# Kernel optimization log

Hardware: AMD Instinct MI355X
Metric: run time of the kernel (lower is better)

Reference implementation:

```python
import jax, jax.numpy as jnp
import numpy as np

N = 2048      # nodes
E = 65536     # edges (avg degree 32)
NV = 6        # n_views (edge_attr dim)
C1, C2, C3 = 32, 32, 32


def _nnconv(x, edge_index, edge_attr, W, b, root, bias, in_c, out_c):
    # Edge MLP: Linear(n_views, in*out) + ReLU -> per-edge weight matrix [E, in, out]
    w = jax.nn.relu(edge_attr @ W + b).reshape(-1, in_c, out_c)
    src, dst = edge_index[0], edge_index[1]  # source_to_target flow
    msg = jnp.einsum('ei,eio->eo', x[src], w)          # gather + edge-specific matmul
    summed = jax.ops.segment_sum(msg, dst, num_segments=N)
    cnt = jax.ops.segment_sum(jnp.ones((msg.shape[0],), x.dtype), dst, num_segments=N)
    agg = summed / jnp.maximum(cnt, 1.0)[:, None]       # scatter-mean (0 for isolated nodes)
    return agg + x @ root + bias                        # root weight + bias (PyG NNConv defaults)


def setup_inputs() -> dict:
    key = jax.random.key(0)
    ks = jax.random.split(key, 12)
    s = 0.1
    return {
        'x': jax.random.normal(ks[0], (N, 1), jnp.float32),
        'edge_attr': jax.random.uniform(ks[1], (E, NV), jnp.float32),
        'edge_index': jax.random.randint(ks[2], (2, E), 0, N, jnp.int64),
        'W1': jax.random.normal(ks[3], (NV, 1 * C1), jnp.float32) * s,
        'b1': jnp.zeros((1 * C1,), jnp.float32),
        'root1': jax.random.normal(ks[4], (1, C1), jnp.float32) * s,
        'bias1': jnp.zeros((C1,), jnp.float32),
        'W2': jax.random.normal(ks[5], (NV, C1 * C2), jnp.float32) * s,
        'b2': jnp.zeros((C1 * C2,), jnp.float32),
        'root2': jax.random.normal(ks[6], (C1, C2), jnp.float32) * s,
        'bias2': jnp.zeros((C2,), jnp.float32),
        'W3': jax.random.normal(ks[7], (NV, C2 * C3), jnp.float32) * s,
        'b3': jnp.zeros((C2 * C3,), jnp.float32),
        'root3': jax.random.normal(ks[8], (C2, C3), jnp.float32) * s,
        'bias3': jnp.zeros((C3,), jnp.float32),
    }


def reference(x, edge_attr, edge_index, W1, b1, root1, bias1, W2, b2, root2, bias2, W3, b3, root3, bias3):
    h = jax.nn.relu(_nnconv(x, edge_index, edge_attr, W1, b1, root1, bias1, 1, C1))
    h = jax.nn.relu(_nnconv(h, edge_index, edge_attr, W2, b2, root2, bias2, C1, C2))
    h = jax.nn.relu(_nnconv(h, edge_index, edge_attr, W3, b3, root3, bias3, C2, C3))
    # CBT: cbt[i, j] = sum_k |h[j, k] - h[i, k]|  (all-pairs L1 distance, [N, N])
    cbt = jnp.sum(jnp.abs(h[None, :, :] - h[:, None, :]), axis=2)
    return cbt
```

## Files before the change

### kernel.cpp

```cpp
#include <hip/hip_runtime.h>

#define N_NODES 2048
#define N_EDGES 65536
#define NV 6
#define C 32
#define BLK 256


__global__ void hist_kernel(const int* __restrict__ dst, int* __restrict__ cnt) {
    int e = blockIdx.x * blockDim.x + threadIdx.x;
    if (e < N_EDGES) atomicAdd(&cnt[dst[e]], 1);
}

__global__ __launch_bounds__(256) void scan_kernel(const int* __restrict__ cnt,
                                                   int* __restrict__ rowptr) {
    __shared__ int part[256];
    const int tid = threadIdx.x;
    int local[8];
    int s = 0;
#pragma unroll
    for (int k = 0; k < 8; k++) { local[k] = cnt[tid * 8 + k]; s += local[k]; }
    part[tid] = s;
    __syncthreads();
    for (int off = 1; off < 256; off <<= 1) {
        int v = (tid >= off) ? part[tid - off] : 0;
        __syncthreads();
        part[tid] += v;
        __syncthreads();
    }
    int run = part[tid] - s;
#pragma unroll
    for (int k = 0; k < 8; k++) { rowptr[tid * 8 + k] = run; run += local[k]; }
    if (tid == 255) rowptr[2048] = run;
}

__global__ void scatter_kernel(const int* __restrict__ dst, const int* __restrict__ rowptr,
                               int* __restrict__ cursor, int* __restrict__ eid) {
    int e = blockIdx.x * blockDim.x + threadIdx.x;
    if (e < N_EDGES) {
        int d = dst[e];
        int pos = atomicAdd(&cursor[d], 1);
        eid[rowptr[d] + pos] = e;
    }
}

__global__ __launch_bounds__(BLK) void layer1_kernel(
    const float* __restrict__ x, const float* __restrict__ ea,
    const int* __restrict__ src, const int* __restrict__ rowptr,
    const int* __restrict__ eid,
    const float* __restrict__ W1, const float* __restrict__ b1,
    const float* __restrict__ root1, const float* __restrict__ bias1,
    float* __restrict__ h1) {
    const int lane = threadIdx.x & 63;
    const int o = lane & 31;
    const int p = lane >> 5;
    const int n = blockIdx.x * 4 + (threadIdx.x >> 6);
    float w1r[NV];
#pragma unroll
    for (int v = 0; v < NV; v++) w1r[v] = W1[v * C + o];
    const float b1o = b1[o];
    const int beg = rowptr[n], end = rowptr[n + 1];
    float acc = 0.0f;
    for (int k = beg + p; k < end; k += 2) {
        const int e = eid[k];
        const float xs = x[src[e]];
        const float* eap = ea + e * NV;
        float t = b1o;
#pragma unroll
        for (int v = 0; v < NV; v++) t = fmaf(eap[v], w1r[v], t);
        acc = fmaf(xs, fmaxf(t, 0.0f), acc);
    }
    acc += __shfl_down(acc, 32);
    if (lane < 32) {
        const float inv = 1.0f / fmaxf((float)(end - beg), 1.0f);
        float r = fmaf(acc, inv, bias1[o]);
        r = fmaf(x[n], root1[o], r);
        h1[n * C + o] = fmaxf(r, 0.0f);
    }
}

__global__ __launch_bounds__(BLK) void edge23_kernel(
    const float* __restrict__ hprev,
    const float* __restrict__ ea,
    const int* __restrict__ src,
    const float* __restrict__ W,
    const float* __restrict__ b,
    float* __restrict__ msg)
{
    __shared__ float hb[4][256];
    const int lane = threadIdx.x & 63;
    const int o = lane & 31;
    const int half = lane >> 5;
    const int i0 = half * 16;
    const int w = threadIdx.x >> 6;
    float* hbw = &hb[w][0];

    float wreg[16][6], breg[16];
#pragma unroll
    for (int j = 0; j < 16; j++) {
#pragma unroll
        for (int v = 0; v < 6; v++) wreg[j][v] = W[v * 1024 + (i0 + j) * C + o];
        breg[j] = b[(i0 + j) * C + o];
    }

    const int wid = (blockIdx.x * BLK + threadIdx.x) >> 6;
    for (int g = wid; g < N_EDGES / 8; g += 2048) {
        const int e0 = g * 8;
        const int4 sq = *(const int4*)&src[e0 + half * 4];
        float4 hq;
        hq.x = hprev[sq.x * C + o];
        hq.y = hprev[sq.y * C + o];
        hq.z = hprev[sq.z * C + o];
        hq.w = hprev[sq.w * C + o];
        *(float4*)&hbw[half * 128 + o * 4] = hq;

        float accs[8];
        const float4* eap4 = (const float4*)(ea + (size_t)e0 * NV);
#pragma unroll
        for (int sub = 0; sub < 2; sub++) {
            float eaf[24];
#pragma unroll
            for (int t = 0; t < 6; t++) *(float4*)&eaf[t * 4] = eap4[sub * 6 + t];
            float a0 = 0.0f, a1 = 0.0f, a2 = 0.0f, a3 = 0.0f;
#pragma unroll
            for (int j = 0; j < 16; j++) {
                const float4 hA = *(const float4*)&hbw[sub * 128 + (i0 + j) * 4];
                const float bb = breg[j];
                const float w0 = wreg[j][0], w1 = wreg[j][1], w2 = wreg[j][2];
                const float w3 = wreg[j][3], w4 = wreg[j][4], w5 = wreg[j][5];
                float t0 = bb, t1 = bb, t2 = bb, t3 = bb;
                t0 = fmaf(eaf[0],  w0, t0); t1 = fmaf(eaf[6],  w0, t1);
                t2 = fmaf(eaf[12], w0, t2); t3 = fmaf(eaf[18], w0, t3);
                t0 = fmaf(eaf[1],  w1, t0); t1 = fmaf(eaf[7],  w1, t1);
                t2 = fmaf(eaf[13], w1, t2); t3 = fmaf(eaf[19], w1, t3);
                t0 = fmaf(eaf[2],  w2, t0); t1 = fmaf(eaf[8],  w2, t1);
                t2 = fmaf(eaf[14], w2, t2); t3 = fmaf(eaf[20], w2, t3);
                t0 = fmaf(eaf[3],  w3, t0); t1 = fmaf(eaf[9],  w3, t1);
                t2 = fmaf(eaf[15], w3, t2); t3 = fmaf(eaf[21], w3, t3);
                t0 = fmaf(eaf[4],  w4, t0); t1 = fmaf(eaf[10], w4, t1);
                t2 = fmaf(eaf[16], w4, t2); t3 = fmaf(eaf[22], w4, t3);
                t0 = fmaf(eaf[5],  w5, t0); t1 = fmaf(eaf[11], w5, t1);
                t2 = fmaf(eaf[17], w5, t2); t3 = fmaf(eaf[23], w5, t3);
                a0 = fmaf(hA.x, fmaxf(t0, 0.0f), a0);
                a1 = fmaf(hA.y, fmaxf(t1, 0.0f), a1);
                a2 = fmaf(hA.z, fmaxf(t2, 0.0f), a2);
                a3 = fmaf(hA.w, fmaxf(t3, 0.0f), a3);
            }
            accs[sub * 4 + 0] = a0; accs[sub * 4 + 1] = a1;
            accs[sub * 4 + 2] = a2; accs[sub * 4 + 3] = a3;
        }
#pragma unroll
        for (int k = 0; k < 8; k++) accs[k] += __shfl_down(accs[k], 32);
        if (lane < 32) {
            float* mp = msg + (size_t)e0 * C + o;
#pragma unroll
            for (int k = 0; k < 8; k++) mp[k * C] = accs[k];
        }
    }
}

__global__ __launch_bounds__(BLK) void gather_kernel(
    const float* __restrict__ msg, const int* __restrict__ rowptr,
    const int* __restrict__ eid, const float* __restrict__ hprev,
    const float* __restrict__ root,
    const float* __restrict__ bias,
    float* __restrict__ hout) {
    const int lane = threadIdx.x & 63;
    const int o = lane & 31;
    const int p = lane >> 5;
    const int n = blockIdx.x * 4 + (threadIdx.x >> 6);
    const int beg = rowptr[n], end = rowptr[n + 1];
    float acc = 0.0f;
    int k = beg + p;
    for (; k + 7 <= end; k += 8) {
        int ka = eid[k], kb = eid[k + 2], kc = eid[k + 4], kd = eid[k + 6];
        float m0 = msg[ka * C + o];
        float m1 = msg[kb * C + o];
        float m2 = msg[kc * C + o];
        float m3 = msg[kd * C + o];
        acc += (m0 + m1) + (m2 + m3);
    }
    for (; k < end; k += 2) acc += msg[eid[k] * C + o];
    acc += __shfl_down(acc, 32);
    if (lane < 32) {
        const float inv = 1.0f / fmaxf((float)(end - beg), 1.0f);
        float r = fmaf(acc, inv, bias[o]);
#pragma unroll
        for (int i = 0; i < C; i++) r = fmaf(hprev[n * C + i], root[i * C + o], r);
        hout[n * C + o] = fmaxf(r, 0.0f);
    }
}

__global__ __launch_bounds__(BLK) void cbt_kernel(const float* __restrict__ h,
                                                  float* __restrict__ out) {
    __shared__ float hj_s[64][33];
    __shared__ float hi_s[64 * 32];
    const int lane = threadIdx.x & 63;
    const int w = threadIdx.x >> 6;
    const int j0 = blockIdx.x * 64;
    const int i0 = blockIdx.y * 64;
    for (int t = threadIdx.x; t < 64 * 32; t += BLK) {
        hj_s[t >> 5][t & 31] = h[j0 * 32 + t];
        hi_s[t] = h[i0 * 32 + t];
    }
    __syncthreads();
    float hj[32];
#pragma unroll
    for (int k = 0; k < 32; k++) hj[k] = hj_s[lane][k];
    const int j = j0 + lane;
#pragma unroll 4
    for (int ii = w * 16; ii < w * 16 + 16; ii++) {
        float acc = 0.0f;
#pragma unroll
        for (int k = 0; k < 32; k++) acc += fabsf(hi_s[ii * 32 + k] - hj[k]);
        out[(size_t)(i0 + ii) * N_NODES + j] = acc;
    }
}

extern "C" void kernel_launch(void* const* d_in, const int* in_sizes, int n_in,
                              void* d_out, int out_size, void* d_ws, size_t ws_size,
                              hipStream_t stream) {
    const float* x         = (const float*)d_in[0];
    const float* edge_attr = (const float*)d_in[1];
    const int*   edge_idx  = (const int*)d_in[2];
    const float* W1 = (const float*)d_in[3];
    const float* b1 = (const float*)d_in[4];
    const float* root1 = (const float*)d_in[5];
    const float* bias1 = (const float*)d_in[6];
    const float* W2 = (const float*)d_in[7];
    const float* b2 = (const float*)d_in[8];
    const float* root2 = (const float*)d_in[9];
    const float* bias2 = (const float*)d_in[10];
    const float* W3 = (const float*)d_in[11];
    const float* b3 = (const float*)d_in[12];
    const float* root3 = (const float*)d_in[13];
    const float* bias3 = (const float*)d_in[14];

    const int* src = edge_idx;
    const int* dst = edge_idx + N_EDGES;

    int* wsi    = (int*)d_ws;
    int* cnt_i  = wsi;
    int* cursor = wsi + 2048;
    int* rowptr = wsi + 4096;
    int* eid    = wsi + 6160;
    float* msg  = (float*)(wsi + 6160 + 65536);
    float* h1   = msg + (size_t)N_EDGES * C;
    float* h2   = h1 + N_NODES * C;
    float* h3   = h2 + N_NODES * C;

    hipMemsetAsync(d_ws, 0, 4096 * sizeof(int), stream);

    hist_kernel<<<N_EDGES / BLK, BLK, 0, stream>>>(dst, cnt_i);
    scan_kernel<<<1, 256, 0, stream>>>(cnt_i, rowptr);
    scatter_kernel<<<N_EDGES / BLK, BLK, 0, stream>>>(dst, rowptr, cursor, eid);

    layer1_kernel<<<N_NODES / 4, BLK, 0, stream>>>(x, edge_attr, src, rowptr, eid,
                                                   W1, b1, root1, bias1, h1);
    edge23_kernel<<<512, BLK, 0, stream>>>(h1, edge_attr, src, W2, b2, msg);
    gather_kernel<<<N_NODES / 4, BLK, 0, stream>>>(msg, rowptr, eid, h1, root2, bias2, h2);
    edge23_kernel<<<512, BLK, 0, stream>>>(h2, edge_attr, src, W3, b3, msg);
    gather_kernel<<<N_NODES / 4, BLK, 0, stream>>>(msg, rowptr, eid, h2, root3, bias3, h3);

    cbt_kernel<<<dim3(N_NODES / 64, N_NODES / 64), BLK, 0, stream>>>(h3, (float*)d_out);
}
```

Baseline: 194.3 us.

## Fuse per-edge message computation with destination-sorted aggregation in layers 2-3

Replaces the edge-parallel message kernel plus gather kernel with a single node-parallel kernel that walks each node's CSR edge list, computes the edge MLP and message in registers and accumulates directly. This removes the E×32 message buffer write and reread and two kernel launches per layer. In exchange, work is split per destination node, so degree imbalance and padded partial groups of 8 edges waste lanes. Edge attributes and source indices are now gathered through eid rather than read contiguously.

Measured after the change: 209.5 us. 7.8% more time.

```diff
diff --git a/kernel.cpp b/kernel.cpp
--- a/kernel.cpp
+++ b/kernel.cpp
@@ -79,13 +79,17 @@
     }
 }
 
-__global__ __launch_bounds__(BLK) void edge23_kernel(
+__global__ __launch_bounds__(BLK, 2) void nnconv23_kernel(
     const float* __restrict__ hprev,
     const float* __restrict__ ea,
     const int* __restrict__ src,
+    const int* __restrict__ rowptr,
+    const int* __restrict__ eid,
     const float* __restrict__ W,
     const float* __restrict__ b,
-    float* __restrict__ msg)
+    const float* __restrict__ root,
+    const float* __restrict__ bias,
+    float* __restrict__ hout)
 {
     __shared__ float hb[4][256];
     const int lane = threadIdx.x & 63;
@@ -94,6 +98,7 @@
     const int i0 = half * 16;
     const int w = threadIdx.x >> 6;
     float* hbw = &hb[w][0];
+    const int n = blockIdx.x * 4 + w;
 
     float wreg[16][6], breg[16];
 #pragma unroll
@@ -103,24 +108,38 @@
         breg[j] = b[(i0 + j) * C + o];
     }
 
-    const int wid = (blockIdx.x * BLK + threadIdx.x) >> 6;
-    for (int g = wid; g < N_EDGES / 8; g += 2048) {
-        const int e0 = g * 8;
-        const int4 sq = *(const int4*)&src[e0 + half * 4];
+    const int beg = rowptr[n], end = rowptr[n + 1];
+    float acc = 0.0f;
+
+    for (int kb = beg; kb < end; kb += 8) {
+        int e[8];
+#pragma unroll
+        for (int k = 0; k < 8; k++) {
+            int kk = kb + k;
+            kk = (kk < end - 1) ? kk : (end - 1);
+            e[k] = __builtin_amdgcn_readfirstlane(eid[kk]);
+        }
+        const int g0 = half ? e[4] : e[0];
+        const int g1 = half ? e[5] : e[1];
+        const int g2 = half ? e[6] : e[2];
+        const int g3 = half ? e[7] : e[3];
+        const int kbase = kb + half * 4;
         float4 hq;
-        hq.x = hprev[sq.x * C + o];
-        hq.y = hprev[sq.y * C + o];
-        hq.z = hprev[sq.z * C + o];
-        hq.w = hprev[sq.w * C + o];
+        hq.x = (kbase + 0 < end) ? hprev[src[g0] * C + o] : 0.0f;
+        hq.y = (kbase + 1 < end) ? hprev[src[g1] * C + o] : 0.0f;
+        hq.z = (kbase + 2 < end) ? hprev[src[g2] * C + o] : 0.0f;
+        hq.w = (kbase + 3 < end) ? hprev[src[g3] * C + o] : 0.0f;
         *(float4*)&hbw[half * 128 + o * 4] = hq;
 
-        float accs[8];
-        const float4* eap4 = (const float4*)(ea + (size_t)e0 * NV);
 #pragma unroll
         for (int sub = 0; sub < 2; sub++) {
             float eaf[24];
 #pragma unroll
-            for (int t = 0; t < 6; t++) *(float4*)&eaf[t * 4] = eap4[sub * 6 + t];
+            for (int k = 0; k < 4; k++) {
+                const float* eap = ea + (size_t)e[sub * 4 + k] * NV;
+#pragma unroll
+                for (int v = 0; v < 6; v++) eaf[k * 6 + v] = eap[v];
+            }
             float a0 = 0.0f, a1 = 0.0f, a2 = 0.0f, a3 = 0.0f;
 #pragma unroll
             for (int j = 0; j < 16; j++) {
@@ -146,41 +165,9 @@
                 a2 = fmaf(hA.z, fmaxf(t2, 0.0f), a2);
                 a3 = fmaf(hA.w, fmaxf(t3, 0.0f), a3);
             }
-            accs[sub * 4 + 0] = a0; accs[sub * 4 + 1] = a1;
-            accs[sub * 4 + 2] = a2; accs[sub * 4 + 3] = a3;
+            acc += (a0 + a1) + (a2 + a3);
         }
-#pragma unroll
-        for (int k = 0; k < 8; k++) accs[k] += __shfl_down(accs[k], 32);
-        if (lane < 32) {
-            float* mp = msg + (size_t)e0 * C + o;
-#pragma unroll
-            for (int k = 0; k < 8; k++) mp[k * C] = accs[k];
-        }
-    }
-}
-
-__global__ __launch_bounds__(BLK) void gather_kernel(
-    const float* __restrict__ msg, const int* __restrict__ rowptr,
-    const int* __restrict__ eid, const float* __restrict__ hprev,
-    const float* __restrict__ root,
-    const float* __restrict__ bias,
-    float* __restrict__ hout) {
-    const int lane = threadIdx.x & 63;
-    const int o = lane & 31;
-    const int p = lane >> 5;
-    const int n = blockIdx.x * 4 + (threadIdx.x >> 6);
-    const int beg = rowptr[n], end = rowptr[n + 1];
-    float acc = 0.0f;
-    int k = beg + p;
-    for (; k + 7 <= end; k += 8) {
-        int ka = eid[k], kb = eid[k + 2], kc = eid[k + 4], kd = eid[k + 6];
-        float m0 = msg[ka * C + o];
-        float m1 = msg[kb * C + o];
-        float m2 = msg[kc * C + o];
-        float m3 = msg[kd * C + o];
-        acc += (m0 + m1) + (m2 + m3);
-    }
-    for (; k < end; k += 2) acc += msg[eid[k] * C + o];
+    }
     acc += __shfl_down(acc, 32);
     if (lane < 32) {
         const float inv = 1.0f / fmaxf((float)(end - beg), 1.0f);
@@ -244,8 +231,7 @@
     int* cursor = wsi + 2048;
     int* rowptr = wsi + 4096;
     int* eid    = wsi + 6160;
-    float* msg  = (float*)(wsi + 6160 + 65536);
-    float* h1   = msg + (size_t)N_EDGES * C;
+    float* h1   = (float*)(wsi + 6160 + 65536);
     float* h2   = h1 + N_NODES * C;
     float* h3   = h2 + N_NODES * C;
 
@@ -257,10 +243,9 @@
 
     layer1_kernel<<<N_NODES / 4, BLK, 0, stream>>>(x, edge_attr, src, rowptr, eid,
                                                    W1, b1, root1, bias1, h1);
-    edge23_kernel<<<512, BLK, 0, stream>>>(h1, edge_attr, src, W2, b2, msg);
-    gather_kernel<<<N_NODES / 4, BLK, 0, stream>>>(msg, rowptr, eid, h1, root2, bias2, h2);
-    edge23_kernel<<<512, BLK, 0, stream>>>(h2, edge_attr, src, W3, b3, msg);
-    gather_kernel<<<N_NODES / 4, BLK, 0, stream>>>(msg, rowptr, eid, h2, root3, bias3, h3);
-
+    nnconv23_kernel<<<N_NODES / 4, BLK, 0, stream>>>(h1, edge_attr, src, rowptr, eid,
+                                                     W2, b2, root2, bias2, h2);
+    nnconv23_kernel<<<N_NODES / 4, BLK, 0, stream>>>(h2, edge_attr, src, rowptr, eid,
+                                                     W3, b3, root3, bias3, h3);
     cbt_kernel<<<dim3(N_NODES / 64, N_NODES / 64), BLK, 0, stream>>>(h3, (float*)d_out);
 }
```
